# Kernel tuning notes

Hardware: AMD Instinct MI355X
Metric: run time of the kernel (lower is better)

## Reference

```python
import jax, jax.numpy as jnp
import numpy as np

B, N_ATOM, COORD = 32, 48, 3
N_ELEM = 4
GRID_SIZE = 128
SIGMA = 0.05      # gaussian broadening of distf
W_SCALE = 1.0     # weightf: exp(-W_SCALE * distance)
INV_SQRT2PI = 1.0 / np.sqrt(2.0 * np.pi)


def _pairs(n):
    # static ordered index pairs i != j (built with numpy -> jit-safe constants)
    ii, jj = np.meshgrid(np.arange(n), np.arange(n), indexing='ij')
    m = ii != jj
    return jnp.asarray(ii[m]), jnp.asarray(jj[m])


def setup_inputs() -> dict:
    key = jax.random.key(0)
    k1, k2 = jax.random.split(key)
    r = jax.random.normal(k1, (B, N_ATOM, COORD), dtype=jnp.float32) * 2.0
    z = jax.random.randint(k2, (N_ATOM,), 0, N_ELEM)  # species index in [0, N_ELEM)
    grid = jnp.linspace(0.0, 2.0, GRID_SIZE, dtype=jnp.float32)
    return {"r": r, "z": z, "grid": grid}


def reference(r, z, grid):
    b, n, c = r.shape
    g = grid.shape[0]
    e = N_ELEM
    dx = grid[1] - grid[0]
    pi, pj = _pairs(n)                              # (P,)

    diff = r[:, pi] - r[:, pj]                      # (b,P,3)
    d = jnp.sqrt(jnp.sum(diff * diff, axis=-1))     # (b,P) pair distances
    gf = 1.0 / d                                    # geomf: inverse distance
    wf = jnp.exp(-W_SCALE * d)                      # weightf: exponential decay
    # distf: normalized gaussian centered at gf, scaled by grid spacing dx
    t = (grid[None, None, :] - gf[..., None]) / SIGMA
    gv = jnp.exp(-0.5 * t * t) * (dx * INV_SQRT2PI / SIGMA)   # (b,P,G)

    contrib = wf[..., None] * gv                    # (b,P,G)
    seg = z[pi] * e + z[pj]                         # (P,) element-pair bucket
    mbtr = jax.ops.segment_sum(contrib.transpose(1, 0, 2), seg, num_segments=e * e)
    mbtr = mbtr.reshape(e, e, b, g).transpose(2, 0, 1, 3)      # (b,E,E,G)

    # analytic divergence wrt the two atoms' coordinates (order=2, coord=3)
    u = diff / d[..., None]                         # dd/dr_i, (b,P,3)
    dd = jnp.stack([u, -u], axis=2)                 # (b,P,2,3): dd/dr_{i}, dd/dr_{j}
    gf_div = -(gf * gf)[..., None, None] * dd       # d(1/d)/dr
    wf_div = -(W_SCALE * wf)[..., None, None] * dd  # d exp(-s d)/dr
    grid_div = gv * (grid[None, None, :] - gf[..., None]) / (SIGMA * SIGMA)  # dgv/dgf

    # (b,P,G,2,3): gv*wf_div + grid_div*gf_div*wf
    div = (gv[:, :, :, None, None] * wf_div[:, :, None, :, :]
           + grid_div[:, :, :, None, None] * (gf_div * wf[..., None, None])[:, :, None, :, :])

    atom_idx = jnp.stack([pi, pj], axis=1)          # (P,2)
    seg_div = (seg[:, None] * n + atom_idx).reshape(-1)        # (2P,) bucket*n + atom
    p2 = div.transpose(1, 3, 0, 2, 4).reshape(-1, b, g, c)     # (2P,b,G,3)
    mbtr_div = jax.ops.segment_sum(p2, seg_div, num_segments=e * e * n)
    mbtr_div = mbtr_div.reshape(e, e, n, b, g, c).transpose(3, 0, 1, 4, 2, 5)  # (b,E,E,G,N,3)
    return mbtr, mbtr_div
```

## Files before the change

kernel.cpp:

```cpp
#include <hip/hip_runtime.h>

#define NB     32
#define NATOM  48
#define NGRID  128
#define KT     8
#define NTHR   384

#define MBTR_ELEMS (NB*16*NGRID)
#define DIV_PER_B  (16*NGRID*NATOM*3)
#define PANE       (NGRID*NATOM*3)
#define MSTRIDE    49

__global__ __launch_bounds__(NTHR)
void mbtr_fused(const float* __restrict__ r, const int* __restrict__ z,
                const float* __restrict__ grid, float* __restrict__ out)
{
    const int kt = blockIdx.x, b = blockIdx.y, t = threadIdx.x;
    const int k0 = kt * KT;

    __shared__ float4 pos_s[NATOM + 1];
    __shared__ int    zl[NATOM];
    __shared__ int    soff_s[5];
    __shared__ float  znpos[NATOM * 3];
    __shared__ float  Mrec[KT * 4 * MSTRIDE];

    if (t < 64) {
        const bool isatom = (t < NATOM);
        int myz = 999;
        float rx = 0.f, ry = 0.f, rz = 0.f;
        if (isatom) {
            myz = z[t];
            zl[t] = myz;
            const float* rp = r + ((size_t)b * NATOM + t) * 3;
            rx = rp[0]; ry = rp[1]; rz = rp[2];
            znpos[t * 3 + 0] = rx; znpos[t * 3 + 1] = ry; znpos[t * 3 + 2] = rz;
        }
        const unsigned long long m0 = __ballot(myz == 0);
        const unsigned long long m1 = __ballot(myz == 1);
        const unsigned long long m2 = __ballot(myz == 2);
        const unsigned long long m3 = __ballot(myz == 3);
        const int c0 = __popcll(m0), c1 = __popcll(m1), c2 = __popcll(m2);
        if (isatom) {
            const unsigned long long mm = (myz == 0) ? m0 : (myz == 1) ? m1
                                        : (myz == 2) ? m2 : m3;
            const int base = (myz == 0) ? 0 : (myz == 1) ? c0
                           : (myz == 2) ? c0 + c1 : c0 + c1 + c2;
            const int rank = __popcll(mm & ((1ull << t) - 1ull));
            pos_s[base + rank] = make_float4(rx, ry, rz, (float)t);
        }
        if (t == 0) {
            soff_s[0] = 0; soff_s[1] = c0; soff_s[2] = c0 + c1;
            soff_s[3] = c0 + c1 + c2; soff_s[4] = NATOM;
            pos_s[NATOM] = make_float4(0.f, 0.f, 0.f, -1.f);
        }
    }
    __syncthreads();

    const int n  = t % NATOM;
    const int kk = t / NATOM;
    const float dx   = grid[1] - grid[0];
    const float coef = dx * 7.9788456080286535f;
    const float mlc  = -__log2f(coef);
    const float isc  = 16.986436005760382f;
    const float tBc  = 23.548200452219559f;
    const float l2e  = 1.4426950408889634f;
    const float gk   = grid[k0 + kk] * isc;
    const float nf   = (float)n;

    float A[4][3] = {{0.f}};
    float M[4]    = {0.f};
    const float rnx = znpos[n * 3 + 0];
    const float rny = znpos[n * 3 + 1];
    const float rnz = znpos[n * 3 + 2];
    const int   zn  = zl[n];
    int so[5];
    #pragma unroll
    for (int e = 0; e < 5; ++e) so[e] = soff_s[e];

    #pragma unroll
    for (int e = 0; e < 4; ++e) {
        #pragma unroll 4
        for (int i = so[e]; i < so[e + 1]; ++i) {
            const float4 rm = pos_s[i];
            const float ddx = rnx - rm.x, ddy = rny - rm.y, ddz = rnz - rm.z;
            float d2 = ddx*ddx + ddy*ddy + ddz*ddz;
            const bool self = (rm.w == nf);
            d2 = self ? 1.0f : d2;
            const float gf  = __builtin_amdgcn_rsqf(d2);
            const float c1  = gf * isc;
            const float d   = d2 * gf;
            float base = fmaf(d, l2e, mlc);
            base = self ? 1e30f : base;
            const float bq  = (gf * gf) * tBc;
            const float tt  = gk - c1;
            const float ex  = exp2f(-fmaf(tt, tt, base));
            M[e] += ex;
            const float p   = ex * fmaf(tt, bq, 1.0f);
            A[e][0] = fmaf(-p, gf * ddx, A[e][0]);
            A[e][1] = fmaf(-p, gf * ddy, A[e][1]);
            A[e][2] = fmaf(-p, gf * ddz, A[e][2]);
        }
    }

    {
        float* mr = Mrec + kk * (4 * MSTRIDE) + n;
        #pragma unroll
        for (int e = 0; e < 4; ++e) mr[e * MSTRIDE] = M[e];
    }

    float* basep = out + MBTR_ELEMS + (size_t)b * DIV_PER_B
                 + (size_t)(k0 + kk) * 144 + n * 3;
    #pragma unroll
    for (int e1 = 0; e1 < 4; ++e1) {
        const bool s1 = (zn == e1);
        #pragma unroll
        for (int e2 = 0; e2 < 4; ++e2) {
            const bool s2 = (zn == e2);
            float3 v;
            v.x = (s1 ? A[e2][0] : 0.f) + (s2 ? A[e1][0] : 0.f);
            v.y = (s1 ? A[e2][1] : 0.f) + (s2 ? A[e1][1] : 0.f);
            v.z = (s1 ? A[e2][2] : 0.f) + (s2 ? A[e1][2] : 0.f);
            *(float3*)(basep + (e1 * 4 + e2) * PANE) = v;
        }
    }

    __syncthreads();

    if (t < 128) {
        const int mpane = t >> 3, mkk = t & 7;
        const int me1 = mpane >> 2, me2 = mpane & 3;
        const float* tr2 = Mrec + mkk * (4 * MSTRIDE) + me2 * MSTRIDE;
        float s = 0.f;
        #pragma unroll
        for (int nn = 0; nn < NATOM; ++nn)
            s += (zl[nn] == me1) ? tr2[nn] : 0.f;
        out[(size_t)b * 2048 + mpane * NGRID + k0 + mkk] = s;
    }
}

extern "C" void kernel_launch(void* const* d_in, const int* in_sizes, int n_in,
                              void* d_out, int out_size, void* d_ws, size_t ws_size,
                              hipStream_t stream)
{
    const float* r    = (const float*)d_in[0];
    const int*   z    = (const int*)  d_in[1];
    const float* grid = (const float*)d_in[2];
    float* out = (float*)d_out;
    (void)d_ws; (void)ws_size;

    mbtr_fused<<<dim3(NGRID / KT, NB), NTHR, 0, stream>>>(r, z, grid, out);
}
```

Baseline: 80.55 us.

## Split element loop across two thread halves to double threads per block

Doubles the block size so that each (atom, grid) point is handled by two threads, each covering two of the four element segments. This halves per-thread serial work and register state for the accumulators. The derivative output write is restructured so that each pane element is written by exactly one half, including zero writes for non-matching panes. The cost is more threads and extra predication in the write phase, and it relies on a launch-bounds occupancy hint.

```diff
diff --git a/kernel.cpp b/kernel.cpp
--- a/kernel.cpp
+++ b/kernel.cpp
@@ -4,14 +4,14 @@
 #define NATOM  48
 #define NGRID  128
 #define KT     8
-#define NTHR   384
+#define NTHR   768
 
 #define MBTR_ELEMS (NB*16*NGRID)
 #define DIV_PER_B  (16*NGRID*NATOM*3)
 #define PANE       (NGRID*NATOM*3)
 #define MSTRIDE    49
 
-__global__ __launch_bounds__(NTHR)
+__global__ __launch_bounds__(NTHR, 6)
 void mbtr_fused(const float* __restrict__ r, const int* __restrict__ z,
                 const float* __restrict__ grid, float* __restrict__ out)
 {
@@ -57,7 +57,8 @@
     __syncthreads();
 
     const int n  = t % NATOM;
-    const int kk = t / NATOM;
+    const int kk = (t / NATOM) & (KT - 1);
+    const int h  = t / (NATOM * KT);
     const float dx   = grid[1] - grid[0];
     const float coef = dx * 7.9788456080286535f;
     const float mlc  = -__log2f(coef);
@@ -67,60 +68,73 @@
     const float gk   = grid[k0 + kk] * isc;
     const float nf   = (float)n;
 
-    float A[4][3] = {{0.f}};
-    float M[4]    = {0.f};
+    float A[2][3] = {{0.f}};
+    float M[2]    = {0.f, 0.f};
     const float rnx = znpos[n * 3 + 0];
     const float rny = znpos[n * 3 + 1];
     const float rnz = znpos[n * 3 + 2];
     const int   zn  = zl[n];
-    int so[5];
-    #pragma unroll
-    for (int e = 0; e < 5; ++e) so[e] = soff_s[e];
+    const int so0 = soff_s[2 * h];
+    const int so1 = soff_s[2 * h + 1];
+    const int so2 = soff_s[2 * h + 2];
 
-    #pragma unroll
-    for (int e = 0; e < 4; ++e) {
-        #pragma unroll 4
-        for (int i = so[e]; i < so[e + 1]; ++i) {
-            const float4 rm = pos_s[i];
-            const float ddx = rnx - rm.x, ddy = rny - rm.y, ddz = rnz - rm.z;
-            float d2 = ddx*ddx + ddy*ddy + ddz*ddz;
-            const bool self = (rm.w == nf);
-            d2 = self ? 1.0f : d2;
-            const float gf  = __builtin_amdgcn_rsqf(d2);
-            const float c1  = gf * isc;
-            const float d   = d2 * gf;
-            float base = fmaf(d, l2e, mlc);
-            base = self ? 1e30f : base;
-            const float bq  = (gf * gf) * tBc;
-            const float tt  = gk - c1;
-            const float ex  = exp2f(-fmaf(tt, tt, base));
-            M[e] += ex;
-            const float p   = ex * fmaf(tt, bq, 1.0f);
-            A[e][0] = fmaf(-p, gf * ddx, A[e][0]);
-            A[e][1] = fmaf(-p, gf * ddy, A[e][1]);
-            A[e][2] = fmaf(-p, gf * ddz, A[e][2]);
-        }
+#define SEG_LOOP(LO, HI, J)                                                 \
+    _Pragma("unroll 4")                                                     \
+    for (int i = (LO); i < (HI); ++i) {                                     \
+        const float4 rm = pos_s[i];      \
+        const float ddx = rnx - rm.x, ddy = rny - rm.y, ddz = rnz - rm.z;   \
+        float d2 = ddx*ddx + ddy*ddy + ddz*ddz;                             \
+        const bool self = (rm.w == nf);                                     \
+        d2 = self ? 1.0f : d2;                           \
+        const float gf  = __builtin_amdgcn_rsqf(d2);               \
+        const float c1  = gf * isc;                                         \
+        const float d   = d2 * gf;                                          \
+        float base = fmaf(d, l2e, mlc);               \
+        base = self ? 1e30f : base;                     \
+        const float bq  = (gf * gf) * tBc;                                  \
+        const float tt  = gk - c1;                                          \
+        const float ex  = exp2f(-fmaf(tt, tt, base));       \
+        M[J] += ex;                                                         \
+        const float p   = ex * fmaf(tt, bq, 1.0f);                          \
+        A[J][0] = fmaf(-p, gf * ddx, A[J][0]);                              \
+        A[J][1] = fmaf(-p, gf * ddy, A[J][1]);                              \
+        A[J][2] = fmaf(-p, gf * ddz, A[J][2]);                              \
     }
+
+    SEG_LOOP(so0, so1, 0)
+    SEG_LOOP(so1, so2, 1)
+#undef SEG_LOOP
 
     {
         float* mr = Mrec + kk * (4 * MSTRIDE) + n;
-        #pragma unroll
-        for (int e = 0; e < 4; ++e) mr[e * MSTRIDE] = M[e];
+        mr[(2 * h + 0) * MSTRIDE] = M[0];
+        mr[(2 * h + 1) * MSTRIDE] = M[1];
     }
 
     float* basep = out + MBTR_ELEMS + (size_t)b * DIV_PER_B
                  + (size_t)(k0 + kk) * 144 + n * 3;
     #pragma unroll
     for (int e1 = 0; e1 < 4; ++e1) {
-        const bool s1 = (zn == e1);
         #pragma unroll
         for (int e2 = 0; e2 < 4; ++e2) {
-            const bool s2 = (zn == e2);
-            float3 v;
-            v.x = (s1 ? A[e2][0] : 0.f) + (s2 ? A[e1][0] : 0.f);
-            v.y = (s1 ? A[e2][1] : 0.f) + (s2 ? A[e1][1] : 0.f);
-            v.z = (s1 ? A[e2][2] : 0.f) + (s2 ? A[e1][2] : 0.f);
-            *(float3*)(basep + (e1 * 4 + e2) * PANE) = v;
+            float3 v; bool w;
+            if (e1 == e2) {
+                w = ((e1 >> 1) == h);
+                const bool s = (zn == e1);
+                v.x = s ? 2.f * A[e1 & 1][0] : 0.f;
+                v.y = s ? 2.f * A[e1 & 1][1] : 0.f;
+                v.z = s ? 2.f * A[e1 & 1][2] : 0.f;
+            } else {
+                const bool o2 = ((e2 >> 1) == h) & (zn == e1);
+                const bool o1 = ((e1 >> 1) == h) & (zn == e2);
+                const bool oz = (h == 0) & (zn != e1) & (zn != e2);
+                w = o2 | o1 | oz;
+                v.x = o2 ? A[e2 & 1][0] : (o1 ? A[e1 & 1][0] : 0.f);
+                v.y = o2 ? A[e2 & 1][1] : (o1 ? A[e1 & 1][1] : 0.f);
+                v.z = o2 ? A[e2 & 1][2] : (o1 ? A[e1 & 1][2] : 0.f);
+            }
+            if (w)
+                *(float3*)(basep + (e1 * 4 + e2) * PANE) = v;
         }
     }
 
```

Result: faster. 78.90 us (-2.0%).
